# Performance work log

Measured on AMD Instinct MI355X. Metric: run time of the kernel, lower is better.

## Reference

```python
import jax, jax.numpy as jnp
import numpy as np

B, L, H, T, C = 64, 1024, 512, 100, 97


def setup_inputs() -> dict:
    key = jax.random.key(0)
    k1, k2, k3, k4, k5 = jax.random.split(key, 5)
    return {
        "position_fmap": jax.random.normal(k1, (B, L, H), dtype=jnp.float32),
        "origin_fmap": jax.random.normal(k2, (B, L, H), dtype=jnp.float32),
        "pos_emb": jax.random.normal(k3, (T, H), dtype=jnp.float32),
        "W_gen": jax.random.normal(k4, (C, H), dtype=jnp.float32) * (1.0 / np.sqrt(H)),
        "b_gen": jax.random.normal(k5, (C,), dtype=jnp.float32) * 0.01,
    }


def reference(position_fmap, origin_fmap, pos_emb, W_gen, b_gen):
    # The torch loop over t in [0, T) computes, per step, scores = fmap @ emb_t,
    # softmax over L, then context = a^T @ origin_fmap. Batched over all steps:
    scores = jnp.einsum('blh,th->btl', position_fmap, pos_emb)   # [B, T, L]
    attn = jax.nn.softmax(scores, axis=-1)                       # softmax over spatial L
    context = jnp.einsum('btl,blh->bth', attn, origin_fmap)      # [B, T, H]
    # generator: Linear(H -> num_classes)
    return jnp.einsum('bth,ch->btc', context, W_gen) + b_gen     # [B, T, C]
```

## Files before the change

kernel.cpp:

```cpp
#include <hip/hip_runtime.h>

#define B_   64
#define L_   1024
#define H_   512
#define T_   100
#define C_   97
#define TP_  112

typedef _Float16 h8 __attribute__((ext_vector_type(8)));
typedef __attribute__((ext_vector_type(4))) float f32x4;

__global__ __launch_bounds__(256) void k0_prep(
    const float* __restrict__ emb, const float* __restrict__ W,
    _Float16* __restrict__ e2, _Float16* __restrict__ w2) {
  const int row = blockIdx.x, tid = threadIdx.x;
  if (row < TP_) {
    for (int j = tid; j < H_; j += 256) {
      float v = (row < T_) ? emb[(size_t)row * H_ + j] : 0.f;
      e2[((size_t)(j >> 3) * TP_ + row) * 8 + (j & 7)] = (_Float16)v;
    }
  } else {
    const int c = row - TP_;
    for (int j = tid; j < H_; j += 256) {
      float v = (c < C_) ? W[(size_t)c * H_ + j] : 0.f;
      w2[((size_t)(j >> 3) * TP_ + c) * 8 + (j & 7)] = (_Float16)v;
    }
  }
}

__device__ __forceinline__ void gl_lds16(const float* g, float* l) {
  __builtin_amdgcn_global_load_lds(
      (const __attribute__((address_space(1))) unsigned int*)g,
      (__attribute__((address_space(3))) unsigned int*)l, 16, 0, 0);
}

__global__ __launch_bounds__(256, 3) void k12_fused(
    const float* __restrict__ fmap, const float* __restrict__ origin,
    const _Float16* __restrict__ e2, const _Float16* __restrict__ w2,
    _Float16* __restrict__ scT, _Float16* __restrict__ GT,
    float* __restrict__ part) {
  __shared__ float sF[2][8][64][4];
  __shared__ float sO[2][8][64][4];
  __shared__ float red_m[4][TP_];
  __shared__ float red_s[4][TP_];
  __shared__ float sMb[TP_];
  const int tid = threadIdx.x;
  const int wave = tid >> 6, lane = tid & 63;
  const int quad = lane >> 4, cc = lane & 15;
  const int b = blockIdx.x >> 4;
  const int lb0 = (blockIdx.x & 15) * 64;
  const int rr = wave * 16 + cc;

  f32x4 accS[7], accG[7];
#pragma unroll
  for (int i = 0; i < 7; ++i) {
    accS[i] = (f32x4){0.f, 0.f, 0.f, 0.f};
    accG[i] = (f32x4){0.f, 0.f, 0.f, 0.f};
  }

  const size_t srow = (size_t)(b * L_ + lb0 + lane) * H_;
  const int u0 = wave * 2, u1 = wave * 2 + 1;
  const _Float16* ep = e2 + (size_t)(quad * TP_ + cc) * 8;
  const _Float16* wp = w2 + (size_t)(quad * TP_ + cc) * 8;

  gl_lds16(fmap   + srow + 0 + u0 * 4, &sF[0][u0][0][0]);
  gl_lds16(fmap   + srow + 0 + u1 * 4, &sF[0][u1][0][0]);
  gl_lds16(origin + srow + 0 + u0 * 4, &sO[0][u0][0][0]);
  gl_lds16(origin + srow + 0 + u1 * 4, &sO[0][u1][0][0]);
  __syncthreads();

#pragma unroll 1
  for (int it = 0; it < 16; ++it) {
    const int k = it * 32;
    const int cur = it & 1;

    const _Float16* ek = ep + (size_t)(k >> 3) * (TP_ * 8);
    const _Float16* wk = wp + (size_t)(k >> 3) * (TP_ * 8);
    h8 ae[7], aw[7];
#pragma unroll
    for (int i = 0; i < 7; ++i) ae[i] = *(const h8*)(ek + i * 128);
#pragma unroll
    for (int i = 0; i < 7; ++i) aw[i] = *(const h8*)(wk + i * 128);

    if (it < 15) {
      const int kn = k + 32;
      const int nb = cur ^ 1;
      gl_lds16(fmap   + srow + kn + u0 * 4, &sF[nb][u0][0][0]);
      gl_lds16(fmap   + srow + kn + u1 * 4, &sF[nb][u1][0][0]);
      gl_lds16(origin + srow + kn + u0 * 4, &sO[nb][u0][0][0]);
      gl_lds16(origin + srow + kn + u1 * 4, &sO[nb][u1][0][0]);
    }

    float4 x0 = *(const float4*)&sF[cur][2 * quad][rr][0];
    float4 x1 = *(const float4*)&sF[cur][2 * quad + 1][rr][0];
    float4 y0 = *(const float4*)&sO[cur][2 * quad][rr][0];
    float4 y1 = *(const float4*)&sO[cur][2 * quad + 1][rr][0];
    h8 bf, bo;
    bf[0] = (_Float16)x0.x; bf[1] = (_Float16)x0.y;
    bf[2] = (_Float16)x0.z; bf[3] = (_Float16)x0.w;
    bf[4] = (_Float16)x1.x; bf[5] = (_Float16)x1.y;
    bf[6] = (_Float16)x1.z; bf[7] = (_Float16)x1.w;
    bo[0] = (_Float16)y0.x; bo[1] = (_Float16)y0.y;
    bo[2] = (_Float16)y0.z; bo[3] = (_Float16)y0.w;
    bo[4] = (_Float16)y1.x; bo[5] = (_Float16)y1.y;
    bo[6] = (_Float16)y1.z; bo[7] = (_Float16)y1.w;

#pragma unroll
    for (int i = 0; i < 7; ++i)
      accS[i] = __builtin_amdgcn_mfma_f32_16x16x32_f16(ae[i], bf, accS[i], 0, 0, 0);
#pragma unroll
    for (int i = 0; i < 7; ++i)
      accG[i] = __builtin_amdgcn_mfma_f32_16x16x32_f16(aw[i], bo, accG[i], 0, 0, 0);

    __syncthreads();
  }

#pragma unroll
  for (int i = 0; i < 7; ++i) {
#pragma unroll
    for (int r = 0; r < 4; ++r) {
      float m = accS[i][r];
#pragma unroll
      for (int d = 1; d < 16; d <<= 1) m = fmaxf(m, __shfl_xor(m, d, 64));
      float e = __expf(accS[i][r] - m);
#pragma unroll
      for (int d = 1; d < 16; d <<= 1) e += __shfl_xor(e, d, 64);
      if (cc == 0) {
        red_m[wave][i * 16 + quad * 4 + r] = m;
        red_s[wave][i * 16 + quad * 4 + r] = e;
      }
    }
  }
  __syncthreads();
  if (tid < TP_) {
    float M = red_m[0][tid], S = red_s[0][tid];
#pragma unroll
    for (int w = 1; w < 4; ++w) {
      float om = red_m[w][tid], os = red_s[w][tid];
      float nM = fmaxf(M, om);
      S = S * __expf(M - nM) + os * __expf(om - nM);
      M = nM;
    }
    float* p = part + ((size_t)blockIdx.x * TP_ + tid) * 2;
    p[0] = M; p[1] = S;
    sMb[tid] = M;
  }
  __syncthreads();

  const int lb = lb0 + rr;
  _Float16* sp = scT + (size_t)b * TP_ * L_ + lb;
  _Float16* gp = GT  + (size_t)b * TP_ * L_ + lb;
#pragma unroll
  for (int i = 0; i < 7; ++i) {
#pragma unroll
    for (int r = 0; r < 4; ++r) {
      const int t = i * 16 + quad * 4 + r;
      sp[(size_t)t * L_] = (_Float16)(accS[i][r] - sMb[t]);
      gp[(size_t)t * L_] = (_Float16)accG[i][r];
    }
  }
}

__global__ __launch_bounds__(512) void k3_out(
    const _Float16* __restrict__ scT, const _Float16* __restrict__ GT,
    const float* __restrict__ part, const float* __restrict__ bias,
    float* __restrict__ out) {
  __shared__ float sAdj[16][16];
  __shared__ float sInv[16];
  __shared__ f32x4 sred[8][4][64];
  const int bid = blockIdx.x;
  const int b = bid / 14;
  const int rem = bid % 14;
  const int mt = rem >> 1;
  const int ng = rem & 1;
  const int NT = ng ? 3 : 4;
  const int ncol0 = ng * 64;
  const int tid = threadIdx.x;
  const int w = tid >> 6, lane = tid & 63;
  const int quad = lane >> 4, cc = lane & 15;

  if (tid < 16) {
    const int t = mt * 16 + tid;
    float mM[16];
    float M = -1e30f, S = 0.f;
#pragma unroll
    for (int s = 0; s < 16; ++s) {
      const float* p = part + ((size_t)(b * 16 + s) * TP_ + t) * 2;
      float om = p[0], os = p[1];
      mM[s] = om;
      float nM = fmaxf(M, om);
      S = S * __expf(M - nM) + os * __expf(om - nM);
      M = nM;
    }
    sInv[tid] = 1.f / S;
#pragma unroll
    for (int s = 0; s < 16; ++s) sAdj[s][tid] = mM[s] - M;
  }
  __syncthreads();

  f32x4 acc[4];
#pragma unroll
  for (int i = 0; i < 4; ++i) acc[i] = (f32x4){0.f, 0.f, 0.f, 0.f};

  const float inv = sInv[cc];
  const _Float16* ap = scT + ((size_t)(b * TP_ + mt * 16 + cc)) * L_ + quad * 8;
  const _Float16* gp = GT  + ((size_t)(b * TP_ + ncol0 + cc)) * L_ + quad * 8;
  const int kbase = w * 128;
#pragma unroll
  for (int l0 = kbase; l0 < kbase + 128; l0 += 32) {
    const float adj = sAdj[(l0 + quad * 8) >> 6][cc];
    h8 v = *(const h8*)(ap + l0);
    h8 a;
#pragma unroll
    for (int j = 0; j < 8; ++j)
      a[j] = (_Float16)(__expf((float)v[j] + adj) * inv);
#pragma unroll
    for (int nt = 0; nt < 4; ++nt) {
      if (nt < NT) {
        h8 bf = *(const h8*)(gp + (size_t)(nt * 16) * L_ + l0);
        acc[nt] = __builtin_amdgcn_mfma_f32_16x16x32_f16(a, bf, acc[nt], 0, 0, 0);
      }
    }
  }

#pragma unroll
  for (int nt = 0; nt < 4; ++nt)
    if (nt < NT) sred[w][nt][lane] = acc[nt];
  __syncthreads();

  if (w < NT) {
    f32x4 s = sred[0][w][lane];
#pragma unroll
    for (int ww = 1; ww < 8; ++ww) s += sred[ww][w][lane];
    const int c = ncol0 + w * 16 + cc;
    if (c < C_) {
      const float bv = bias[c];
#pragma unroll
      for (int r = 0; r < 4; ++r) {
        const int t = mt * 16 + quad * 4 + r;
        if (t < T_) out[((size_t)b * T_ + t) * C_ + c] = s[r] + bv;
      }
    }
  }
}

extern "C" void kernel_launch(void* const* d_in, const int* in_sizes, int n_in,
                              void* d_out, int out_size, void* d_ws, size_t ws_size,
                              hipStream_t stream) {
  const float* fmap   = (const float*)d_in[0];
  const float* origin = (const float*)d_in[1];
  const float* emb    = (const float*)d_in[2];
  const float* W      = (const float*)d_in[3];
  const float* bias   = (const float*)d_in[4];
  float* out = (float*)d_out;

  char* ws = (char*)d_ws;
  _Float16* e2   = (_Float16*)(ws);
  _Float16* w2   = (_Float16*)(ws + 114688);
  _Float16* scT  = (_Float16*)(ws + 229376);
  float*    part = (float*)   (ws + 14909440);
  _Float16* GT   = (_Float16*)(ws + 15826944);

  hipLaunchKernelGGL(k0_prep,   dim3(224),  dim3(256), 0, stream, emb, W, e2, w2);
  hipLaunchKernelGGL(k12_fused, dim3(1024), dim3(256), 0, stream,
                     fmap, origin, e2, w2, scT, GT, part);
  hipLaunchKernelGGL(k3_out,    dim3(896),  dim3(512), 0, stream,
                     scT, GT, part, bias, out);
}
```

Before: 336.3 us.

## Coalesce fmap/origin staging loads with XOR-swizzled LDS layout, raise occupancy hint

Reorganizes the global-to-LDS staging so each wave's 64 lanes load 8 contiguous rows of 128 bytes instead of 64 strided rows, improving global-memory coalescing. The LDS tile becomes row-major [row][chunk][4] with an XOR swizzle on the chunk index so the MFMA-operand reads avoid bank conflicts. It also raises the launch_bounds minimum blocks per CU from 3 to 4, which may constrain registers and cause spills.

```diff
diff --git a/kernel.cpp b/kernel.cpp
--- a/kernel.cpp
+++ b/kernel.cpp
@@ -34,13 +34,13 @@
       (__attribute__((address_space(3))) unsigned int*)l, 16, 0, 0);
 }
 
-__global__ __launch_bounds__(256, 3) void k12_fused(
+__global__ __launch_bounds__(256, 4) void k12_fused(
     const float* __restrict__ fmap, const float* __restrict__ origin,
     const _Float16* __restrict__ e2, const _Float16* __restrict__ w2,
     _Float16* __restrict__ scT, _Float16* __restrict__ GT,
     float* __restrict__ part) {
-  __shared__ float sF[2][8][64][4];
-  __shared__ float sO[2][8][64][4];
+  __shared__ float sF[2][64][8][4];
+  __shared__ float sO[2][64][8][4];
   __shared__ float red_m[4][TP_];
   __shared__ float red_s[4][TP_];
   __shared__ float sMb[TP_];
@@ -58,15 +58,25 @@
     accG[i] = (f32x4){0.f, 0.f, 0.f, 0.f};
   }
 
-  const size_t srow = (size_t)(b * L_ + lb0 + lane) * H_;
-  const int u0 = wave * 2, u1 = wave * 2 + 1;
+  const int s0 = wave * 128 + lane;
+  const int r0 = s0 >> 3;
+  const int c0 = (s0 & 7) ^ (r0 & 7);
+  const int r1 = r0 + 8;
+  const int c1 = (s0 & 7) ^ (r1 & 7);
+  const float* gf0 = fmap   + (size_t)(b * L_ + lb0 + r0) * H_ + c0 * 4;
+  const float* gf1 = fmap   + (size_t)(b * L_ + lb0 + r1) * H_ + c1 * 4;
+  const float* go0 = origin + (size_t)(b * L_ + lb0 + r0) * H_ + c0 * 4;
+  const float* go1 = origin + (size_t)(b * L_ + lb0 + r1) * H_ + c1 * 4;
+  const int d0 = wave * 512;
+  const int d1 = wave * 512 + 256;
+
   const _Float16* ep = e2 + (size_t)(quad * TP_ + cc) * 8;
   const _Float16* wp = w2 + (size_t)(quad * TP_ + cc) * 8;
 
-  gl_lds16(fmap   + srow + 0 + u0 * 4, &sF[0][u0][0][0]);
-  gl_lds16(fmap   + srow + 0 + u1 * 4, &sF[0][u1][0][0]);
-  gl_lds16(origin + srow + 0 + u0 * 4, &sO[0][u0][0][0]);
-  gl_lds16(origin + srow + 0 + u1 * 4, &sO[0][u1][0][0]);
+  gl_lds16(gf0, &sF[0][0][0][0] + d0);
+  gl_lds16(gf1, &sF[0][0][0][0] + d1);
+  gl_lds16(go0, &sO[0][0][0][0] + d0);
+  gl_lds16(go1, &sO[0][0][0][0] + d1);
   __syncthreads();
 
 #pragma unroll 1
@@ -85,16 +95,17 @@
     if (it < 15) {
       const int kn = k + 32;
       const int nb = cur ^ 1;
-      gl_lds16(fmap   + srow + kn + u0 * 4, &sF[nb][u0][0][0]);
-      gl_lds16(fmap   + srow + kn + u1 * 4, &sF[nb][u1][0][0]);
-      gl_lds16(origin + srow + kn + u0 * 4, &sO[nb][u0][0][0]);
-      gl_lds16(origin + srow + kn + u1 * 4, &sO[nb][u1][0][0]);
-    }
-
-    float4 x0 = *(const float4*)&sF[cur][2 * quad][rr][0];
-    float4 x1 = *(const float4*)&sF[cur][2 * quad + 1][rr][0];
-    float4 y0 = *(const float4*)&sO[cur][2 * quad][rr][0];
-    float4 y1 = *(const float4*)&sO[cur][2 * quad + 1][rr][0];
+      gl_lds16(gf0 + kn, &sF[nb][0][0][0] + d0);
+      gl_lds16(gf1 + kn, &sF[nb][0][0][0] + d1);
+      gl_lds16(go0 + kn, &sO[nb][0][0][0] + d0);
+      gl_lds16(go1 + kn, &sO[nb][0][0][0] + d1);
+    }
+
+    const int e_ = rr & 7;
+    float4 x0 = *(const float4*)&sF[cur][rr][(2 * quad) ^ e_][0];
+    float4 x1 = *(const float4*)&sF[cur][rr][(2 * quad + 1) ^ e_][0];
+    float4 y0 = *(const float4*)&sO[cur][rr][(2 * quad) ^ e_][0];
+    float4 y1 = *(const float4*)&sO[cur][rr][(2 * quad + 1) ^ e_][0];
     h8 bf, bo;
     bf[0] = (_Float16)x0.x; bf[1] = (_Float16)x0.y;
     bf[2] = (_Float16)x0.z; bf[3] = (_Float16)x0.w;
```

Result: slower. 349.3 us (+3.8%).
